# Performance work log

Measured on AMD Instinct MI355X. Metric: run time of the kernel, lower is better.

Reference implementation:

```python
import jax, jax.numpy as jnp
import numpy as np

B, S, E, H = 4, 2048, 1024, 16
D = E // H  # head dim = 64


def setup_inputs() -> dict:
    key = jax.random.key(0)
    ks = jax.random.split(key, 5)
    scale = 0.02
    return {
        "x": jax.random.normal(ks[0], (B, S, E), dtype=jnp.float32),
        "Wa_w": jax.random.normal(ks[1], (3 * E, E), dtype=jnp.float32) * scale,
        "Wa_b": jax.random.normal(ks[2], (3 * E,), dtype=jnp.float32) * scale,
        "Wo_w": jax.random.normal(ks[3], (E, E), dtype=jnp.float32) * scale,
        "Wo_b": jax.random.normal(ks[4], (E,), dtype=jnp.float32) * scale,
    }


def reference(x, Wa_w, Wa_b, Wo_w, Wo_b):
    b, s, e = x.shape
    # Fused QKV projection (torch Linear: x @ W^T + b)
    qkv = jnp.einsum("bse,fe->bsf", x, Wa_w) + Wa_b  # [B,S,3E]
    q, k, v = jnp.split(qkv, 3, axis=-1)
    # [B,S,E] -> [B,H,S,D]
    def heads(t):
        return t.reshape(b, s, H, D).transpose(0, 2, 1, 3)
    q, k, v = heads(q), heads(k), heads(v)
    # Causal attention with explicit score matrix (as in the original)
    scores = jnp.einsum("bhqd,bhkd->bhqk", q, k) / jnp.sqrt(jnp.float32(D))
    causal = jnp.tril(jnp.ones((s, s), dtype=bool))
    scores = jnp.where(causal, scores, -jnp.inf)
    attn = jax.nn.softmax(scores, axis=-1)  # dropout p=0 -> identity
    out = jnp.einsum("bhqk,bhkd->bhqd", attn, v)  # [B,H,S,D]
    out = out.transpose(0, 2, 1, 3).reshape(b, s, e)
    return jnp.einsum("bse,fe->bsf", out, Wo_w) + Wo_b
```

## Files before the change

kernel.cpp:

```cpp
#include <hip/hip_runtime.h>
#include <hip/hip_bf16.h>
#include <cstdint>

typedef __bf16 bf16_t;
typedef __attribute__((ext_vector_type(8))) __bf16 bf16x8;
typedef __attribute__((ext_vector_type(4))) __bf16 bf16x4;
typedef __attribute__((ext_vector_type(4))) float f32x4;

#define B_ 4
#define S_ 2048
#define E_ 1024
#define H_ 16
#define D_ 64

#define QSCALE 0.18033688011112042f

__global__ void cvt_f32_to_bf16(const float* __restrict__ in, bf16_t* __restrict__ out, int n4) {
    int i = blockIdx.x * blockDim.x + threadIdx.x;
    int stride = gridDim.x * blockDim.x;
    for (; i < n4; i += stride) {
        f32x4 v = reinterpret_cast<const f32x4*>(in)[i];
        bf16x4 o;
        o.x = (bf16_t)v.x; o.y = (bf16_t)v.y; o.z = (bf16_t)v.z; o.w = (bf16_t)v.w;
        reinterpret_cast<bf16x4*>(out)[i] = o;
    }
}

__device__ __forceinline__ void gload_lds16(const bf16_t* g, bf16_t* l) {
    __builtin_amdgcn_global_load_lds((const __attribute__((address_space(1))) void*)g,
                                     (__attribute__((address_space(3))) void*)l, 16, 0, 0);
}

__device__ __forceinline__ void wait_vm4() { asm volatile("s_waitcnt vmcnt(4)" ::: "memory"); }
__device__ __forceinline__ void wait_vm0() { asm volatile("s_waitcnt vmcnt(0)" ::: "memory"); }

template <int MODE>
__launch_bounds__(256, 3)
__global__ void gemm_pipe(const bf16_t* __restrict__ A, const bf16_t* __restrict__ Bm,
                          const float* __restrict__ bias,
                          int M, int N,
                          bf16_t* __restrict__ Qg, bf16_t* __restrict__ Kg,
                          bf16_t* __restrict__ Vtg, float* __restrict__ Outf) {
    constexpr int K = 1024, BK = 32, NKT = K / BK;
    constexpr int BM = 128, BN = 128;
    __shared__ __align__(16) bf16_t As[3][BM * BK];
    __shared__ __align__(16) bf16_t Bs[3][BN * BK];

    const int nwg = gridDim.x;
    const int cpx = nwg >> 3;
    const int bid = (blockIdx.x & 7) * cpx + (blockIdx.x >> 3);

    const int nTN = N / BN;
    const int mt = bid / nTN, nt = bid % nTN;
    const int m0 = mt * BM, n0 = nt * BN;

    const int t = threadIdx.x;
    const int lane = t & 63;
    const int wid = t >> 6;
    const int wr = wid >> 1, wc = wid & 1;
    const int lr = lane & 15, lg = lane >> 4;

    auto mkSrc = [&](const bf16_t* base, int c, int row0) {
        const int line = c >> 3, chg = (c & 7) ^ (line & 7);
        return base + (int64_t)(row0 + 2 * line + (chg >> 2)) * K + (chg & 3) * 8;
    };
    const bf16_t* aSrc0 = mkSrc(A, t, m0);
    const bf16_t* aSrc1 = mkSrc(A, t + 256, m0);
    const bf16_t* bSrc0 = mkSrc(Bm, t, n0);
    const bf16_t* bSrc1 = mkSrc(Bm, t + 256, n0);

    auto stageT = [&](int kt, int buf) {
        gload_lds16(aSrc0 + kt * BK, &As[buf][t * 8]);
        gload_lds16(aSrc1 + kt * BK, &As[buf][(t + 256) * 8]);
        gload_lds16(bSrc0 + kt * BK, &Bs[buf][t * 8]);
        gload_lds16(bSrc1 + kt * BK, &Bs[buf][(t + 256) * 8]);
    };

    auto fragOff = [](int row, int kc) -> int {
        const int line = row >> 1;
        const int ch = ((row & 1) << 2) | kc;
        return line * 64 + ((ch ^ (line & 7)) << 3);
    };

    f32x4 acc[4][4] = {};

    stageT(0, 0);
    stageT(1, 1);

    int bufc = 0, bufs = 2;
    for (int kt = 0; kt < NKT; ++kt) {
        if (kt < NKT - 1) wait_vm4(); else wait_vm0();
        __builtin_amdgcn_s_barrier();
        __builtin_amdgcn_sched_barrier(0);

        if (kt + 2 < NKT) stageT(kt + 2, bufs);

        bf16x8 bfr[4], afr[4];
#pragma unroll
        for (int j = 0; j < 4; ++j)
            bfr[j] = *(const bf16x8*)&Bs[bufc][fragOff(wc * 64 + j * 16 + lr, lg)];
#pragma unroll
        for (int i = 0; i < 4; ++i)
            afr[i] = *(const bf16x8*)&As[bufc][fragOff(wr * 64 + i * 16 + lr, lg)];

        __builtin_amdgcn_s_setprio(1);
#pragma unroll
        for (int i = 0; i < 4; ++i)
#pragma unroll
            for (int j = 0; j < 4; ++j)
                acc[i][j] = __builtin_amdgcn_mfma_f32_16x16x32_bf16(afr[i], bfr[j], acc[i][j], 0, 0, 0);
        __builtin_amdgcn_s_setprio(0);

        bufc = (bufc == 2) ? 0 : bufc + 1;
        bufs = (bufs == 2) ? 0 : bufs + 1;
    }

    if (MODE == 0) {
        const int which = n0 >> 10;
#pragma unroll
        for (int j = 0; j < 4; ++j) {
            const int f = n0 + wc * 64 + j * 16 + lr;
            const float bv = bias[f];
            const int fe = f - which * E_;
            const int h = fe >> 6, d = fe & 63;
#pragma unroll
            for (int i = 0; i < 4; ++i) {
#pragma unroll
                for (int r = 0; r < 4; ++r) {
                    const int m = m0 + wr * 64 + i * 16 + lg * 4 + r;
                    const int b = m >> 11, si = m & (S_ - 1);
                    const float v = acc[i][j][r] + bv;
                    if (which == 0)
                        Qg[(((int64_t)(b * H_ + h)) * S_ + si) * D_ + d] = (bf16_t)(v * QSCALE);
                    else if (which == 1)
                        Kg[(((int64_t)(b * H_ + h)) * S_ + si) * D_ + d] = (bf16_t)v;
                    else
                        Vtg[(((int64_t)(b * H_ + h)) * D_ + d) * S_ + si] = (bf16_t)v;
                }
            }
        }
    } else {
#pragma unroll
        for (int j = 0; j < 4; ++j) {
            const int f = n0 + wc * 64 + j * 16 + lr;
            const float bv = bias[f];
#pragma unroll
            for (int i = 0; i < 4; ++i) {
#pragma unroll
                for (int r = 0; r < 4; ++r) {
                    const int m = m0 + wr * 64 + i * 16 + lg * 4 + r;
                    Outf[(int64_t)m * N + f] = acc[i][j][r] + bv;
                }
            }
        }
    }
}

__launch_bounds__(256, 4)
__global__ void attn_causal(const bf16_t* __restrict__ Qg, const bf16_t* __restrict__ Kg,
                            const bf16_t* __restrict__ Vtg, bf16_t* __restrict__ Og) {
    __shared__ __align__(16) bf16_t Ks[2][64 * 64];
    __shared__ __align__(16) bf16_t Vs[2][64 * 64];
    __shared__ __align__(16) bf16_t P_lds[4][16 * 64];

    const int bid = blockIdx.x;
    const int xcd = bid & 7, j = bid >> 3;
    const int bh = (j >> 4) * 8 + xcd;
    const int i = j & 15;
    const int qtA = i, qtB = 31 - i;

    const int t = threadIdx.x, lane = t & 63, w = t >> 6;
    const int lr = lane & 15, lg = lane >> 4;
    const int q0A = qtA * 64 + w * 16;
    const int q0B = qtB * 64 + w * 16;

    const bf16_t* Qb = Qg + (int64_t)bh * S_ * D_;
    const bf16_t* Kb = Kg + (int64_t)bh * S_ * D_;
    const bf16_t* Vb = Vtg + (int64_t)bh * D_ * S_;

    const int srow = t >> 3;
    const int scol_sw = (t & 7) ^ (srow & 7);

    auto stageK = [&](int buf, int kv0) {
        const bf16_t* base = Kb + (kv0 + srow) * D_ + scol_sw * 8;
        gload_lds16(base, &Ks[buf][t * 8]);
        gload_lds16(base + 32 * D_, &Ks[buf][t * 8 + 2048]);
    };
    auto stageV = [&](int buf, int kv0) {
        const bf16_t* base = Vb + srow * S_ + kv0 + scol_sw * 8;
        gload_lds16(base, &Vs[buf][t * 8]);
        gload_lds16(base + 32 * S_, &Vs[buf][t * 8 + 2048]);
    };

    auto psw = [](int row, int col) {
        return row * 64 + ((((col >> 3) ^ (row & 7)) << 3) | (col & 7));
    };

    bf16x8 qfA[2], qfB[2];
#pragma unroll
    for (int kk = 0; kk < 2; ++kk) {
        qfA[kk] = *(const bf16x8*)&Qb[(q0A + lr) * D_ + kk * 32 + lg * 8];
        qfB[kk] = *(const bf16x8*)&Qb[(q0B + lr) * D_ + kk * 32 + lg * 8];
    }

    bf16x8 ones;
#pragma unroll
    for (int e = 0; e < 8; ++e) ones[e] = (bf16_t)1.0f;

    f32x4 oA[4] = {}, oB[4] = {};
    f32x4 lA = {}, lB = {};

    int cur = 0;
    stageK(0, 0);
    stageV(0, 0);
    __syncthreads();

    for (int tkv = 0; tkv <= qtB; ++tkv) {
        const int kv0 = tkv * 64;
        if (tkv < qtB) { stageK(cur ^ 1, kv0 + 64); stageV(cur ^ 1, kv0 + 64); }

        auto process = [&](int q0, const bf16x8* qf, f32x4* o, f32x4& accl, bf16_t* Pw) {
            f32x4 sc[4] = {};
            __builtin_amdgcn_s_setprio(1);
#pragma unroll
            for (int nj = 0; nj < 4; ++nj) {
                if (kv0 + nj * 16 <= q0 + 15) {
                    const int krow = nj * 16 + lr;
#pragma unroll
                    for (int kk = 0; kk < 2; ++kk) {
                        bf16x8 kfr = *(const bf16x8*)&Ks[cur][krow * 64 + (((kk * 4 + lg) ^ (krow & 7)) * 8)];
                        sc[nj] = __builtin_amdgcn_mfma_f32_16x16x32_bf16(qf[kk], kfr, sc[nj], 0, 0, 0);
                    }
                }
            }
            __builtin_amdgcn_s_setprio(0);

            if (kv0 + 64 > q0) {
#pragma unroll
                for (int nj = 0; nj < 4; ++nj) {
                    const int col = kv0 + nj * 16 + lr;
#pragma unroll
                    for (int r = 0; r < 4; ++r) {
                        const int rowg = q0 + lg * 4 + r;
                        if (col > rowg) sc[nj][r] = -1e30f;
                    }
                }
            }

#pragma unroll
            for (int nj = 0; nj < 4; ++nj)
#pragma unroll
                for (int r = 0; r < 4; ++r)
                    Pw[psw(lg * 4 + r, nj * 16 + lr)] = (bf16_t)__builtin_amdgcn_exp2f(sc[nj][r]);
            asm volatile("s_waitcnt lgkmcnt(0)" ::: "memory");
            __builtin_amdgcn_sched_barrier(0);

            __builtin_amdgcn_s_setprio(1);
#pragma unroll
            for (int kk = 0; kk < 2; ++kk) {
                bf16x8 pa = *(const bf16x8*)&Pw[psw(lr, kk * 32 + lg * 8)];
                accl = __builtin_amdgcn_mfma_f32_16x16x32_bf16(pa, ones, accl, 0, 0, 0);
#pragma unroll
                for (int nd = 0; nd < 4; ++nd) {
                    const int vrow = nd * 16 + lr;
                    bf16x8 vf = *(const bf16x8*)&Vs[cur][vrow * 64 + (((kk * 4 + lg) ^ (vrow & 7)) * 8)];
                    o[nd] = __builtin_amdgcn_mfma_f32_16x16x32_bf16(pa, vf, o[nd], 0, 0, 0);
                }
            }
            __builtin_amdgcn_s_setprio(0);
        };

        process(q0B, qfB, oB, lB, &P_lds[w][0]);
        if (tkv <= qtA) process(q0A, qfA, oA, lA, &P_lds[w][0]);

        __syncthreads();
        cur ^= 1;
    }

    const int b = bh >> 4, h = bh & 15;
#pragma unroll
    for (int r = 0; r < 4; ++r) {
        const float rlA = 1.0f / lA[r];
        const float rlB = 1.0f / lB[r];
        const int rA = q0A + lg * 4 + r;
        const int rB = q0B + lg * 4 + r;
#pragma unroll
        for (int nd = 0; nd < 4; ++nd) {
            Og[((int64_t)(b * S_ + rA)) * E_ + h * D_ + nd * 16 + lr] = (bf16_t)(oA[nd][r] * rlA);
            Og[((int64_t)(b * S_ + rB)) * E_ + h * D_ + nd * 16 + lr] = (bf16_t)(oB[nd][r] * rlB);
        }
    }
}

extern "C" void kernel_launch(void* const* d_in, const int* in_sizes, int n_in,
                              void* d_out, int out_size, void* d_ws, size_t ws_size,
                              hipStream_t stream) {
    const float* x    = (const float*)d_in[0];
    const float* Wa_w = (const float*)d_in[1];
    const float* Wa_b = (const float*)d_in[2];
    const float* Wo_w = (const float*)d_in[3];
    const float* Wo_b = (const float*)d_in[4];
    float* out = (float*)d_out;

    const size_t M = (size_t)B_ * S_;
    char* ws = (char*)d_ws;
    bf16_t* xb  = (bf16_t*)ws; ws += M * E_ * 2;
    bf16_t* wab = (bf16_t*)ws; ws += (size_t)3 * E_ * E_ * 2;
    bf16_t* wob = (bf16_t*)ws; ws += (size_t)E_ * E_ * 2;
    bf16_t* Qg  = (bf16_t*)ws; ws += M * E_ * 2;
    bf16_t* Kg  = (bf16_t*)ws; ws += M * E_ * 2;
    bf16_t* Vtg = (bf16_t*)ws; ws += M * E_ * 2;
    bf16_t* Og  = (bf16_t*)ws; ws += M * E_ * 2;

    cvt_f32_to_bf16<<<2048, 256, 0, stream>>>(x, xb, (int)(M * E_ / 4));
    cvt_f32_to_bf16<<<768, 256, 0, stream>>>(Wa_w, wab, 3 * E_ * E_ / 4);
    cvt_f32_to_bf16<<<256, 256, 0, stream>>>(Wo_w, wob, E_ * E_ / 4);

    gemm_pipe<0><<<1536, 256, 0, stream>>>(
        xb, wab, Wa_b, 8192, 3072, Qg, Kg, Vtg, nullptr);

    attn_causal<<<B_ * H_ * 16, 256, 0, stream>>>(Qg, Kg, Vtg, Og);

    gemm_pipe<1><<<512, 256, 0, stream>>>(
        Og, wob, Wo_b, 8192, 1024, nullptr, nullptr, nullptr, out);
}
```

Measured before the change: 190.6 us.

## Process four query tiles per attention block to reuse staged K/V tiles

```diff
diff --git a/kernel.cpp b/kernel.cpp
--- a/kernel.cpp
+++ b/kernel.cpp
@@ -156,23 +156,21 @@
     }
 }
 
-__launch_bounds__(256, 4)
+__launch_bounds__(256, 2)
 __global__ void attn_causal(const bf16_t* __restrict__ Qg, const bf16_t* __restrict__ Kg,
                             const bf16_t* __restrict__ Vtg, bf16_t* __restrict__ Og) {
     __shared__ __align__(16) bf16_t Ks[2][64 * 64];
     __shared__ __align__(16) bf16_t Vs[2][64 * 64];
-    __shared__ __align__(16) bf16_t P_lds[4][16 * 64];
+    __shared__ __align__(16) bf16_t P_lds[16][16 * 64];
 
     const int bid = blockIdx.x;
     const int xcd = bid & 7, j = bid >> 3;
-    const int bh = (j >> 4) * 8 + xcd;
-    const int i = j & 15;
-    const int qtA = i, qtB = 31 - i;
+    const int bh = (j >> 3) * 8 + xcd;
+    const int i = j & 7;
+    const int qts[4] = {i, 15 - i, 16 + i, 31 - i};
 
     const int t = threadIdx.x, lane = t & 63, w = t >> 6;
     const int lr = lane & 15, lg = lane >> 4;
-    const int q0A = qtA * 64 + w * 16;
-    const int q0B = qtB * 64 + w * 16;
 
     const bf16_t* Qb = Qg + (int64_t)bh * S_ * D_;
     const bf16_t* Kb = Kg + (int64_t)bh * S_ * D_;
@@ -196,30 +194,34 @@
         return row * 64 + ((((col >> 3) ^ (row & 7)) << 3) | (col & 7));
     };
 
-    bf16x8 qfA[2], qfB[2];
-#pragma unroll
-    for (int kk = 0; kk < 2; ++kk) {
-        qfA[kk] = *(const bf16x8*)&Qb[(q0A + lr) * D_ + kk * 32 + lg * 8];
-        qfB[kk] = *(const bf16x8*)&Qb[(q0B + lr) * D_ + kk * 32 + lg * 8];
+    int q0s[4];
+    bf16x8 qf[4][2];
+#pragma unroll
+    for (int s = 0; s < 4; ++s) {
+        q0s[s] = qts[s] * 64 + w * 16;
+#pragma unroll
+        for (int kk = 0; kk < 2; ++kk)
+            qf[s][kk] = *(const bf16x8*)&Qb[(q0s[s] + lr) * D_ + kk * 32 + lg * 8];
     }
 
     bf16x8 ones;
 #pragma unroll
     for (int e = 0; e < 8; ++e) ones[e] = (bf16_t)1.0f;
 
-    f32x4 oA[4] = {}, oB[4] = {};
-    f32x4 lA = {}, lB = {};
-
+    f32x4 o[4][4] = {};
+    f32x4 l[4] = {};
+
+    const int lastT = qts[3];
     int cur = 0;
     stageK(0, 0);
     stageV(0, 0);
     __syncthreads();
 
-    for (int tkv = 0; tkv <= qtB; ++tkv) {
+    for (int tkv = 0; tkv <= lastT; ++tkv) {
         const int kv0 = tkv * 64;
-        if (tkv < qtB) { stageK(cur ^ 1, kv0 + 64); stageV(cur ^ 1, kv0 + 64); }
-
-        auto process = [&](int q0, const bf16x8* qf, f32x4* o, f32x4& accl, bf16_t* Pw) {
+        if (tkv < lastT) { stageK(cur ^ 1, kv0 + 64); stageV(cur ^ 1, kv0 + 64); }
+
+        auto process = [&](int q0, const bf16x8* qfs, f32x4* os, f32x4& accl, bf16_t* Pw) {
             f32x4 sc[4] = {};
             __builtin_amdgcn_s_setprio(1);
 #pragma unroll
@@ -229,7 +231,7 @@
 #pragma unroll
                     for (int kk = 0; kk < 2; ++kk) {
                         bf16x8 kfr = *(const bf16x8*)&Ks[cur][krow * 64 + (((kk * 4 + lg) ^ (krow & 7)) * 8)];
-                        sc[nj] = __builtin_amdgcn_mfma_f32_16x16x32_bf16(qf[kk], kfr, sc[nj], 0, 0, 0);
+                        sc[nj] = __builtin_amdgcn_mfma_f32_16x16x32_bf16(qfs[kk], kfr, sc[nj], 0, 0, 0);
                     }
                 }
             }
@@ -264,14 +266,16 @@
                 for (int nd = 0; nd < 4; ++nd) {
                     const int vrow = nd * 16 + lr;
                     bf16x8 vf = *(const bf16x8*)&Vs[cur][vrow * 64 + (((kk * 4 + lg) ^ (vrow & 7)) * 8)];
-                    o[nd] = __builtin_amdgcn_mfma_f32_16x16x32_bf16(pa, vf, o[nd], 0, 0, 0);
+                    os[nd] = __builtin_amdgcn_mfma_f32_16x16x32_bf16(pa, vf, os[nd], 0, 0, 0);
                 }
             }
             __builtin_amdgcn_s_setprio(0);
         };
 
-        process(q0B, qfB, oB, lB, &P_lds[w][0]);
-        if (tkv <= qtA) process(q0A, qfA, oA, lA, &P_lds[w][0]);
+#pragma unroll
+        for (int s = 3; s >= 0; --s)
+            if (tkv <= qts[s])
+                process(q0s[s], qf[s], o[s], l[s], &P_lds[w * 4 + s][0]);
 
         __syncthreads();
         cur ^= 1;
@@ -279,15 +283,15 @@
 
     const int b = bh >> 4, h = bh & 15;
 #pragma unroll
-    for (int r = 0; r < 4; ++r) {
-        const float rlA = 1.0f / lA[r];
-        const float rlB = 1.0f / lB[r];
-        const int rA = q0A + lg * 4 + r;
-        const int rB = q0B + lg * 4 + r;
-#pragma unroll
-        for (int nd = 0; nd < 4; ++nd) {
-            Og[((int64_t)(b * S_ + rA)) * E_ + h * D_ + nd * 16 + lr] = (bf16_t)(oA[nd][r] * rlA);
-            Og[((int64_t)(b * S_ + rB)) * E_ + h * D_ + nd * 16 + lr] = (bf16_t)(oB[nd][r] * rlB);
+    for (int s = 0; s < 4; ++s) {
+#pragma unroll
+        for (int r = 0; r < 4; ++r) {
+            const float rl = 1.0f / l[s][r];
+            const int rowg = q0s[s] + lg * 4 + r;
+#pragma unroll
+            for (int nd = 0; nd < 4; ++nd)
+                Og[((int64_t)(b * S_ + rowg)) * E_ + h * D_ + nd * 16 + lr] =
+                    (bf16_t)(o[s][nd][r] * rl);
         }
     }
 }
@@ -319,7 +323,7 @@
     gemm_pipe<0><<<1536, 256, 0, stream>>>(
         xb, wab, Wa_b, 8192, 3072, Qg, Kg, Vtg, nullptr);
 
-    attn_causal<<<B_ * H_ * 16, 256, 0, stream>>>(Qg, Kg, Vtg, Og);
+    attn_causal<<<B_ * H_ * 8, 256, 0, stream>>>(Qg, Kg, Vtg, Og);
 
     gemm_pipe<1><<<512, 256, 0, stream>>>(
         Og, wob, Wo_b, 8192, 1024, nullptr, nullptr, nullptr, out);
```

New measurement: 197.3 us. 3.5% more time.
